# Kernel tuning notes

Measured on AMD Instinct MI355X. Metric: run time of the kernel, lower is better.

The kernel has to match this reference:

```python
import jax, jax.numpy as jnp
import numpy as np

B, C, N, T, H = 4, 128, 512, 16, 4
DK = C // H
SCALE = float(np.sqrt(DK) * 1.0)  # dk**0.5 * max(tau,1e-6), tau=1.0


def setup_inputs() -> dict:
    key = jax.random.key(0)
    ks = jax.random.split(key, 6)
    x = jax.random.normal(ks[0], (B, C, N, T), jnp.float32)
    Wq = jax.random.normal(ks[1], (C, C), jnp.float32) * (1.0 / np.sqrt(C))
    Wk = jax.random.normal(ks[2], (C, C), jnp.float32) * (1.0 / np.sqrt(C))
    # original init is identity; add tiny noise so it's not degenerate
    structural = jnp.eye(N, dtype=jnp.float32) + 0.01 * jax.random.normal(ks[3], (N, N), jnp.float32)
    fusion_w = jax.random.normal(ks[4], (2,), jnp.float32) * 0.5  # 1x1 conv over 2 input channels
    fusion_b = (jax.random.normal(ks[5], (), jnp.float32) * 0.1)
    return {"x": x, "Wq": Wq, "Wk": Wk, "structural": structural,
            "fusion_w": fusion_w, "fusion_b": fusion_b}


def reference(x, Wq, Wk, structural, fusion_w, fusion_b):
    # x: [B, C, N, T]. 1x1 conv == per-channel linear; arrange to [B,T,N,H,DK]
    Q = jnp.einsum('oc,bcnt->btno', Wq, x).reshape(B, T, N, H, DK)
    K = jnp.einsum('oc,bcnt->btno', Wk, x).reshape(B, T, N, H, DK)
    # scores: [B, T, H, N, N]
    scores = jnp.einsum('btnhd,btmhd->bthnm', Q, K) / SCALE
    att_node = jax.nn.softmax(scores, axis=-1).mean(axis=(1, 2))  # [B, N, N]
    att_struct = jax.nn.softmax(structural, axis=-1)              # [N, N]
    # fusion conv (1x1, 2->1 channels) == weighted sum + bias
    fused = fusion_w[0] * att_node + fusion_w[1] * att_struct[None] + fusion_b
    fused = 0.5 * (fused + jnp.swapaxes(fused, 1, 2))  # symmetrize
    fused = jax.nn.softmax(fused, axis=-1)             # normalize='softmax'
    x_bt = jnp.transpose(x, (0, 3, 2, 1))              # [B, T, N, C]
    x_att = jnp.einsum('bij,btjc->btic', fused, x_bt)  # weighted aggregation over nodes
    return jnp.transpose(x_att, (0, 3, 2, 1))          # [B, C, N, T]
```

## Files before the change

### kernel.cpp

```cpp
#include <hip/hip_runtime.h>

#define GPART 8
#define INV_SCALE 0.17677669529663687f
#define SMEM_SZ 36864

typedef __attribute__((ext_vector_type(8))) short bf16x8;
typedef __attribute__((ext_vector_type(4))) float f32x4;

__device__ __forceinline__ unsigned int pk2bf(float a, float b) {
  unsigned int ua = __float_as_uint(a);
  ua = (ua + 0x7FFFu + ((ua >> 16) & 1u)) >> 16;
  unsigned int ub = __float_as_uint(b);
  ub = (ub + 0x7FFFu + ((ub >> 16) & 1u)) >> 16;
  return ua | (ub << 16);
}
__device__ __forceinline__ ushort cv1(float f) {
  unsigned int u = __float_as_uint(f);
  return (ushort)((u + 0x7FFFu + ((u >> 16) & 1u)) >> 16);
}
__device__ __forceinline__ unsigned int pkfast(float a, float b) {
  unsigned int au = __float_as_uint(a) + 0x8000u;
  unsigned int bu = __float_as_uint(b) + 0x8000u;
  return __builtin_amdgcn_perm(bu, au, 0x07060302u);
}
__device__ __forceinline__ float bf2f(ushort v) {
  return __uint_as_float((unsigned int)v << 16);
}

__device__ __forceinline__ float blk_max(float v, float* red, int tid) {
#pragma unroll
  for (int off = 32; off > 0; off >>= 1) v = fmaxf(v, __shfl_xor(v, off, 64));
  if ((tid & 63) == 0) red[tid >> 6] = v;
  __syncthreads();
  v = fmaxf(fmaxf(red[0], red[1]), fmaxf(red[2], red[3]));
  __syncthreads();
  return v;
}
__device__ __forceinline__ float blk_sum(float v, float* red, int tid) {
#pragma unroll
  for (int off = 32; off > 0; off >>= 1) v += __shfl_xor(v, off, 64);
  if ((tid & 63) == 0) red[tid >> 6] = v;
  __syncthreads();
  v = (red[0] + red[1]) + (red[2] + red[3]);
  __syncthreads();
  return v;
}

__global__ __launch_bounds__(256) void k_ph1(const float* __restrict__ x,
                                             const float* __restrict__ Wq,
                                             const float* __restrict__ Wk,
                                             const float* __restrict__ S,
                                             ushort* __restrict__ Qb,
                                             ushort* __restrict__ Kb,
                                             float* __restrict__ st) {
  __shared__ __align__(16) char smem[SMEM_SZ];
  float* xl = (float*)smem;
  const int bid = blockIdx.x;
  const int b = bid >> 7;
  const int nt0 = (bid & 127) * 64;
  const int nq = nt0 >> 4;
  const int tid = threadIdx.x;
  const int w = tid >> 6, lane = tid & 63;
  const int lm = lane & 15, quad = lane >> 4;

  const float* xb = x + (size_t)b * 1048576 + nt0;
#pragma unroll
  for (int L = tid * 4; L < 8192; L += 1024) {
    int c = L >> 6, j = L & 63;
    float4 v = *(const float4*)(xb + c * 8192 + j);
    float2* dp = (float2*)(xl + c * 66 + j);
    dp[0] = make_float2(v.x, v.y);
    dp[1] = make_float2(v.z, v.w);
  }

  const int o0 = w * 32;
  bf16x8 aq[2][4], ak[2][4];
#pragma unroll
  for (int ot = 0; ot < 2; ++ot)
#pragma unroll
    for (int kc = 0; kc < 4; ++kc) {
      const int off = (o0 + ot * 16 + lm) * 128 + kc * 32 + quad * 8;
      const float4 q1 = *(const float4*)(Wq + off);
      const float4 q2 = *(const float4*)(Wq + off + 4);
      const float4 k1 = *(const float4*)(Wk + off);
      const float4 k2 = *(const float4*)(Wk + off + 4);
      union { uint4 u; bf16x8 v; } cq, ck;
      cq.u.x = pk2bf(q1.x * INV_SCALE, q1.y * INV_SCALE);
      cq.u.y = pk2bf(q1.z * INV_SCALE, q1.w * INV_SCALE);
      cq.u.z = pk2bf(q2.x * INV_SCALE, q2.y * INV_SCALE);
      cq.u.w = pk2bf(q2.z * INV_SCALE, q2.w * INV_SCALE);
      ck.u.x = pk2bf(k1.x, k1.y);
      ck.u.y = pk2bf(k1.z, k1.w);
      ck.u.z = pk2bf(k2.x, k2.y);
      ck.u.w = pk2bf(k2.z, k2.w);
      aq[ot][kc] = cq.v;
      ak[ot][kc] = ck.v;
    }
  __syncthreads();

#pragma unroll
  for (int jtl = 0; jtl < 4; ++jtl) {
    bf16x8 bfr[4];
#pragma unroll
    for (int kc = 0; kc < 4; ++kc) {
      const float* sp = xl + (kc * 32 + quad * 8) * 66 + jtl * 16 + lm;
      float f0 = sp[0],   f1 = sp[66],  f2 = sp[132], f3 = sp[198];
      float f4 = sp[264], f5 = sp[330], f6 = sp[396], f7 = sp[462];
      union { uint4 u; bf16x8 v; } cv;
      cv.u.x = pkfast(f0, f1);
      cv.u.y = pkfast(f2, f3);
      cv.u.z = pkfast(f4, f5);
      cv.u.w = pkfast(f6, f7);
      bfr[kc] = cv.v;
    }

    f32x4 accq0 = {0,0,0,0}, accq1 = {0,0,0,0};
    f32x4 acck0 = {0,0,0,0}, acck1 = {0,0,0,0};
#pragma unroll
    for (int kc = 0; kc < 4; ++kc) {
      accq0 = __builtin_amdgcn_mfma_f32_16x16x32_bf16(aq[0][kc], bfr[kc], accq0, 0, 0, 0);
      accq1 = __builtin_amdgcn_mfma_f32_16x16x32_bf16(aq[1][kc], bfr[kc], accq1, 0, 0, 0);
      acck0 = __builtin_amdgcn_mfma_f32_16x16x32_bf16(ak[0][kc], bfr[kc], acck0, 0, 0, 0);
      acck1 = __builtin_amdgcn_mfma_f32_16x16x32_bf16(ak[1][kc], bfr[kc], acck1, 0, 0, 0);
    }

    const size_t base = (size_t)b * 1048576 + (size_t)lm * 65536 + w * 16384 +
                        (size_t)(nq + jtl) * 32 + quad * 4;
    uint2 uq0, uq1, uk0, uk1;
    uq0.x = pk2bf(accq0[0], accq0[1]); uq0.y = pk2bf(accq0[2], accq0[3]);
    uq1.x = pk2bf(accq1[0], accq1[1]); uq1.y = pk2bf(accq1[2], accq1[3]);
    uk0.x = pk2bf(acck0[0], acck0[1]); uk0.y = pk2bf(acck0[2], acck0[3]);
    uk1.x = pk2bf(acck1[0], acck1[1]); uk1.y = pk2bf(acck1[2], acck1[3]);
    *(uint2*)(Qb + base)      = uq0;
    *(uint2*)(Qb + base + 16) = uq1;
    *(uint2*)(Kb + base)      = uk0;
    *(uint2*)(Kb + base + 16) = uk1;
  }

  {
    float* red = (float*)(smem + 34816);
    __syncthreads();
    const int i = bid;
    float s0 = S[i * 512 + tid], s1 = S[i * 512 + tid + 256];
    float m = blk_max(fmaxf(s0, s1), red, tid);
    float e0 = __expf(s0 - m), e1 = __expf(s1 - m);
    float sum = blk_sum(e0 + e1, red, tid);
    float inv = 1.0f / sum;
    st[i * 512 + tid] = e0 * inv;
    st[i * 512 + tid + 256] = e1 * inv;
  }
}

__global__ __launch_bounds__(256, 4) void k_ph2(const ushort* __restrict__ Qb,
                                                const ushort* __restrict__ Kb,
                                                ushort* __restrict__ part) {
  __shared__ float SH[16 * 516];
  __shared__ float red[2][4][16];
  const int strip = blockIdx.x, g = blockIdx.y, b = blockIdx.z;
  const int tid = threadIdx.x;
  const int w = tid >> 6, lane = tid & 63;
  const int lm = lane & 15, quad = lane >> 4;
  const int n0 = strip * 16;
  const int wcol0 = w * 128;

  float acc[32];
#pragma unroll
  for (int i = 0; i < 32; ++i) acc[i] = 0.f;

  for (int pi = 0; pi < 8; ++pi) {
    const int p = (g << 3) + pi;
    const size_t base = (size_t)((b * 16 + (p >> 2)) * 4 + (p & 3)) * 16384;
    bf16x8 afrag = *(const bf16x8*)(Qb + base + (size_t)(n0 + lm) * 32 + quad * 8);
    bf16x8 bfr[8];
#pragma unroll
    for (int ct = 0; ct < 8; ++ct)
      bfr[ct] = *(const bf16x8*)(Kb + base + (size_t)(wcol0 + ct * 16 + lm) * 32 + quad * 8);

    f32x4 d[8];
#pragma unroll
    for (int ct = 0; ct < 8; ++ct) {
      f32x4 z = {0.f, 0.f, 0.f, 0.f};
      d[ct] = __builtin_amdgcn_mfma_f32_16x16x32_bf16(afrag, bfr[ct], z, 0, 0, 0);
    }

    float cur[32];
    float rp0 = 0.f, rp1 = 0.f, rp2 = 0.f, rp3 = 0.f;
#pragma unroll
    for (int ct = 0; ct < 8; ++ct) {
      float e0 = __expf(d[ct][0]);
      float e1 = __expf(d[ct][1]);
      float e2 = __expf(d[ct][2]);
      float e3 = __expf(d[ct][3]);
      cur[ct * 4 + 0] = e0; cur[ct * 4 + 1] = e1;
      cur[ct * 4 + 2] = e2; cur[ct * 4 + 3] = e3;
      rp0 += e0; rp1 += e1; rp2 += e2; rp3 += e3;
    }
#pragma unroll
    for (int m = 1; m < 16; m <<= 1) {
      rp0 += __shfl_xor(rp0, m);
      rp1 += __shfl_xor(rp1, m);
      rp2 += __shfl_xor(rp2, m);
      rp3 += __shfl_xor(rp3, m);
    }
    if (lm == 0) {
      red[pi & 1][w][quad * 4 + 0] = rp0;
      red[pi & 1][w][quad * 4 + 1] = rp1;
      red[pi & 1][w][quad * 4 + 2] = rp2;
      red[pi & 1][w][quad * 4 + 3] = rp3;
    }
    __syncthreads();
#pragma unroll
    for (int r = 0; r < 4; ++r) {
      float rs = red[pi & 1][0][quad * 4 + r] + red[pi & 1][1][quad * 4 + r] +
                 red[pi & 1][2][quad * 4 + r] + red[pi & 1][3][quad * 4 + r];
      float inv = 1.0f / rs;
#pragma unroll
      for (int ct = 0; ct < 8; ++ct)
        acc[ct * 4 + r] = fmaf(cur[ct * 4 + r], inv, acc[ct * 4 + r]);
    }
  }

#pragma unroll
  for (int ct = 0; ct < 8; ++ct) {
#pragma unroll
    for (int r = 0; r < 4; ++r)
      SH[(quad * 4 + r) * 516 + wcol0 + ct * 16 + lm] = acc[ct * 4 + r];
  }
  __syncthreads();
  const int row = tid >> 4, colb = (tid & 15) * 4;
  ushort* po = part + ((size_t)((g * 4 + b) * 512 + n0 + row)) * 512 + colb;
#pragma unroll
  for (int k = 0; k < 8; ++k) {
    f32x4 v = *(const f32x4*)(SH + row * 516 + colb + k * 64);
    uint2 u;
    u.x = pk2bf(v[0], v[1]);
    u.y = pk2bf(v[2], v[3]);
    *(uint2*)(po + k * 64) = u;
  }
}

__global__ __launch_bounds__(256) void k_ph3(const float* __restrict__ x,
                                             ushort* __restrict__ xtb,
                                             const ushort* __restrict__ part,
                                             float* __restrict__ Ssym,
                                             float* __restrict__ st) {
  __shared__ __align__(16) char smem[SMEM_SZ];
  const int bid = blockIdx.x;
  const int tid = threadIdx.x;

  {
    ushort* xs = (ushort*)smem;
    const int c = bid & 127, b = bid >> 7;
    const float* in = x + ((size_t)b * 128 + c) * 8192;
    ushort* outp = xtb + ((size_t)b * 128 + c) * 8192;
#pragma unroll
    for (int it = 0; it < 8; ++it) {
      int idx = (tid + it * 256) * 4;
      int j = idx >> 4, t0 = idx & 15;
      float4 v = *(const float4*)(in + idx);
      xs[(t0 + 0) * 520 + j] = cv1(v.x);
      xs[(t0 + 1) * 520 + j] = cv1(v.y);
      xs[(t0 + 2) * 520 + j] = cv1(v.z);
      xs[(t0 + 3) * 520 + j] = cv1(v.w);
    }
    __syncthreads();
#pragma unroll
    for (int it = 0; it < 4; ++it) {
      int u = (tid + it * 256) * 8;
      int t = u >> 9, j0 = u & 511;
      *(uint4*)(outp + u) = *(const uint4*)(xs + t * 520 + j0);
    }
  }
  __syncthreads();

  if (bid < 180) {
    float* L1 = (float*)smem;
    float* L2 = L1 + 64 * 68;
    const int z = bid / 36;
    int rem = bid % 36, ti = 0;
    for (;;) { int cnt = 8 - ti; if (rem < cnt) break; rem -= cnt; ++ti; }
    const int tj = ti + rem;
    const bool diag = (ti == tj);
    const int rr = tid >> 2, cc = (tid & 3) * 16;

    float a1[16], a2[16];
#pragma unroll
    for (int k = 0; k < 16; ++k) { a1[k] = 0.f; a2[k] = 0.f; }

    if (z == 4) {
      const float* p1 = st + (ti * 64 + rr) * 512 + tj * 64 + cc;
      const float* p2 = st + (tj * 64 + rr) * 512 + ti * 64 + cc;
#pragma unroll
      for (int q = 0; q < 4; ++q) {
        float4 v = *(const float4*)(p1 + q * 4);
        a1[q * 4 + 0] = v.x; a1[q * 4 + 1] = v.y;
        a1[q * 4 + 2] = v.z; a1[q * 4 + 3] = v.w;
        if (!diag) {
          float4 u = *(const float4*)(p2 + q * 4);
          a2[q * 4 + 0] = u.x; a2[q * 4 + 1] = u.y;
          a2[q * 4 + 2] = u.z; a2[q * 4 + 3] = u.w;
        }
      }
    } else {
      const int b = z;
#pragma unroll
      for (int g = 0; g < GPART; ++g) {
        const ushort* p1 = part + ((size_t)((g * 4 + b) * 512 + ti * 64 + rr)) * 512 + tj * 64 + cc;
        const ushort* p2 = part + ((size_t)((g * 4 + b) * 512 + tj * 64 + rr)) * 512 + ti * 64 + cc;
#pragma unroll
        for (int q = 0; q < 4; ++q) {
          ushort4 v = *(const ushort4*)(p1 + q * 4);
          a1[q * 4 + 0] += bf2f(v.x); a1[q * 4 + 1] += bf2f(v.y);
          a1[q * 4 + 2] += bf2f(v.z); a1[q * 4 + 3] += bf2f(v.w);
          if (!diag) {
            ushort4 u = *(const ushort4*)(p2 + q * 4);
            a2[q * 4 + 0] += bf2f(u.x); a2[q * 4 + 1] += bf2f(u.y);
            a2[q * 4 + 2] += bf2f(u.z); a2[q * 4 + 3] += bf2f(u.w);
          }
        }
      }
    }

#pragma unroll
    for (int q = 0; q < 4; ++q) {
      *(float4*)(L1 + rr * 68 + cc + q * 4) =
          make_float4(a1[q * 4], a1[q * 4 + 1], a1[q * 4 + 2], a1[q * 4 + 3]);
      if (!diag)
        *(float4*)(L2 + rr * 68 + cc + q * 4) =
            make_float4(a2[q * 4], a2[q * 4 + 1], a2[q * 4 + 2], a2[q * 4 + 3]);
    }
    __syncthreads();

    float* M = (z < 4) ? (Ssym + (size_t)z * 262144) : st;
    const float* LT = diag ? L1 : L2;
#pragma unroll
    for (int q = 0; q < 4; ++q) {
      const int c = cc + q * 4;
      float4 o;
      o.x = L1[rr * 68 + c + 0] + LT[(c + 0) * 68 + rr];
      o.y = L1[rr * 68 + c + 1] + LT[(c + 1) * 68 + rr];
      o.z = L1[rr * 68 + c + 2] + LT[(c + 2) * 68 + rr];
      o.w = L1[rr * 68 + c + 3] + LT[(c + 3) * 68 + rr];
      *(float4*)(M + (ti * 64 + rr) * 512 + tj * 64 + c) = o;
    }
    if (!diag) {
#pragma unroll
      for (int q = 0; q < 4; ++q) {
        const int c = cc + q * 4;
        float4 o;
        o.x = L2[rr * 68 + c + 0] + L1[(c + 0) * 68 + rr];
        o.y = L2[rr * 68 + c + 1] + L1[(c + 1) * 68 + rr];
        o.z = L2[rr * 68 + c + 2] + L1[(c + 2) * 68 + rr];
        o.w = L2[rr * 68 + c + 3] + L1[(c + 3) * 68 + rr];
        *(float4*)(M + (tj * 64 + rr) * 512 + ti * 64 + c) = o;
      }
    }
  }
}

__global__ __launch_bounds__(256) void k_ph4(const float* __restrict__ Ssym,
                                             const float* __restrict__ st,
                                             const float* __restrict__ fw,
                                             const float* __restrict__ fb,
                                             ushort* __restrict__ fusedb) {
  __shared__ float red[4];
  const int i = blockIdx.x, tid = threadIdx.x;
  const float w0s = fw[0] * (0.5f / 64.f);
  const float w1s = fw[1] * 0.5f;
  const float bias = fb[0];
  float2 s2 = *(const float2*)(st + (size_t)i * 512 + tid * 2);
  for (int b = 0; b < 4; ++b) {
    const float* A = Ssym + (size_t)b * 262144 + (size_t)i * 512;
    float2 a2 = *(const float2*)(A + tid * 2);
    float l0 = fmaf(w0s, a2.x, fmaf(w1s, s2.x, bias));
    float l1 = fmaf(w0s, a2.y, fmaf(w1s, s2.y, bias));
    float m = blk_max(fmaxf(l0, l1), red, tid);
    float e0 = __expf(l0 - m), e1 = __expf(l1 - m);
    float sum = blk_sum(e0 + e1, red, tid);
    float inv = 1.0f / sum;
    *(unsigned int*)(fusedb + ((size_t)(b * 512 + i)) * 512 + tid * 2) =
        pk2bf(e0 * inv, e1 * inv);
  }
}

__global__ __launch_bounds__(256) void k_ph5(const ushort* __restrict__ fusedb,
                                             const ushort* __restrict__ xtb,
                                             float* __restrict__ out) {
  __shared__ ushort xs[16 * 520];
  const int cg = blockIdx.x;
  const int i0 = blockIdx.y * 64;
  const int b = blockIdx.z;
  const int tid = threadIdx.x, w = tid >> 6, lane = tid & 63;
  const int lm = lane & 15, quad = lane >> 4;

  const ushort* fr = fusedb + ((size_t)(b * 512 + i0 + w * 16 + lm)) * 512 + quad * 8;
  bf16x8 af[16];
#pragma unroll
  for (int kk = 0; kk < 16; ++kk) af[kk] = *(const bf16x8*)(fr + kk * 32);

  const ushort* xg = xtb + ((size_t)b * 128 + cg * 8) * 8192;
  uint4 rg[4];
#pragma unroll
  for (int it = 0; it < 4; ++it) rg[it] = *(const uint4*)(xg + (tid + it * 256) * 8);

  for (int c = 0; c < 8; ++c) {
#pragma unroll
    for (int it = 0; it < 4; ++it) {
      int u = (tid + it * 256) * 8;
      int t = u >> 9, j0 = u & 511;
      *(uint4*)(xs + t * 520 + j0) = rg[it];
    }
    __syncthreads();
    if (c < 7) {
      const ushort* xg2 = xg + (size_t)(c + 1) * 8192;
#pragma unroll
      for (int it = 0; it < 4; ++it) rg[it] = *(const uint4*)(xg2 + (tid + it * 256) * 8);
    }
    f32x4 acc = {0.f, 0.f, 0.f, 0.f};
#pragma unroll
    for (int kk = 0; kk < 16; ++kk) {
      bf16x8 bf = *(const bf16x8*)(xs + lm * 520 + kk * 32 + quad * 8);
      acc = __builtin_amdgcn_mfma_f32_16x16x32_bf16(af[kk], bf, acc, 0, 0, 0);
    }
    float* op = out + (size_t)b * 1048576 + (size_t)(cg * 8 + c) * 8192 +
                (size_t)(i0 + w * 16 + quad * 4) * 16 + lm;
    op[0]  = acc[0];
    op[16] = acc[1];
    op[32] = acc[2];
    op[48] = acc[3];
    __syncthreads();
  }
}

extern "C" void kernel_launch(void* const* d_in, const int* in_sizes, int n_in,
                              void* d_out, int out_size, void* d_ws, size_t ws_size,
                              hipStream_t stream) {
  const float* x  = (const float*)d_in[0];
  const float* Wq = (const float*)d_in[1];
  const float* Wk = (const float*)d_in[2];
  const float* S  = (const float*)d_in[3];
  const float* fw = (const float*)d_in[4];
  const float* fb = (const float*)d_in[5];
  float* out = (float*)d_out;

  ushort* Qb   = (ushort*)d_ws;
  ushort* Kb   = Qb + 4194304;
  ushort* part = Kb + 4194304;
  ushort* xtb  = Qb;
  float* Ssym  = (float*)(part + 8388608);
  float* st    = Ssym + 1048576;
  ushort* fusedb = (ushort*)(st + 262144);

  k_ph1<<<dim3(512),          256, 0, stream>>>(x, Wq, Wk, S, Qb, Kb, st);
  k_ph2<<<dim3(32, GPART, 4), 256, 0, stream>>>(Qb, Kb, part);
  k_ph3<<<dim3(512),          256, 0, stream>>>(x, xtb, part, Ssym, st);
  k_ph4<<<dim3(512),          256, 0, stream>>>(Ssym, st, fw, fb, fusedb);
  k_ph5<<<dim3(16, 8, 4),     256, 0, stream>>>(fusedb, xtb, out);
}
```

Measured before the change: 163.6 us.

## Fuse fusion-softmax into aggregation GEMM and move x transpose into score kernel

The x-to-bf16 transpose moves from the symmetrize kernel into the score-partials kernel, so the symmetrize kernel now launches only its 180 needed blocks. The separate fusion-softmax kernel is removed. The aggregation kernel now computes exp of the fused logits directly into its bf16 MFMA A-fragments. It normalizes each output row by the reciprocal row sum after the GEMM, and skips the max subtraction because the logits are small. This saves one launch and the bf16 fused-matrix round trip through memory. In exchange, every channel-group block re-reads the fp32 Ssym and st rows and recomputes the exps, a 16x redundancy that will mostly hit L2.

```diff
diff --git a/kernel.cpp b/kernel.cpp
--- a/kernel.cpp
+++ b/kernel.cpp
@@ -153,13 +153,43 @@
 
 __global__ __launch_bounds__(256, 4) void k_ph2(const ushort* __restrict__ Qb,
                                                 const ushort* __restrict__ Kb,
+                                                const float* __restrict__ x,
+                                                ushort* __restrict__ xtb,
                                                 ushort* __restrict__ part) {
-  __shared__ float SH[16 * 516];
-  __shared__ float red[2][4][16];
+  __shared__ __align__(16) char smem[SMEM_SZ];
   const int strip = blockIdx.x, g = blockIdx.y, b = blockIdx.z;
+  const int flat = strip + 32 * g + 256 * b;
   const int tid = threadIdx.x;
   const int w = tid >> 6, lane = tid & 63;
   const int lm = lane & 15, quad = lane >> 4;
+
+  if (flat < 512) {
+    ushort* xs = (ushort*)smem;
+    const int cc = flat & 127, bc = flat >> 7;
+    const float* in = x + ((size_t)bc * 128 + cc) * 8192;
+    ushort* outp = xtb + ((size_t)bc * 128 + cc) * 8192;
+#pragma unroll
+    for (int it = 0; it < 8; ++it) {
+      int idx = (tid + it * 256) * 4;
+      int j = idx >> 4, t0 = idx & 15;
+      float4 v = *(const float4*)(in + idx);
+      xs[(t0 + 0) * 520 + j] = cv1(v.x);
+      xs[(t0 + 1) * 520 + j] = cv1(v.y);
+      xs[(t0 + 2) * 520 + j] = cv1(v.z);
+      xs[(t0 + 3) * 520 + j] = cv1(v.w);
+    }
+    __syncthreads();
+#pragma unroll
+    for (int it = 0; it < 4; ++it) {
+      int u = (tid + it * 256) * 8;
+      int t = u >> 9, j0 = u & 511;
+      *(uint4*)(outp + u) = *(const uint4*)(xs + t * 520 + j0);
+    }
+  }
+  __syncthreads();
+
+  float* SH = (float*)smem;
+  float (*red)[4][16] = (float(*)[4][16])(smem + 33024);
   const int n0 = strip * 16;
   const int wcol0 = w * 128;
 
@@ -239,164 +269,142 @@
   }
 }
 
-__global__ __launch_bounds__(256) void k_ph3(const float* __restrict__ x,
-                                             ushort* __restrict__ xtb,
-                                             const ushort* __restrict__ part,
+__global__ __launch_bounds__(256) void k_ph3(const ushort* __restrict__ part,
                                              float* __restrict__ Ssym,
                                              float* __restrict__ st) {
   __shared__ __align__(16) char smem[SMEM_SZ];
   const int bid = blockIdx.x;
   const int tid = threadIdx.x;
-
-  {
-    ushort* xs = (ushort*)smem;
-    const int c = bid & 127, b = bid >> 7;
-    const float* in = x + ((size_t)b * 128 + c) * 8192;
-    ushort* outp = xtb + ((size_t)b * 128 + c) * 8192;
-#pragma unroll
-    for (int it = 0; it < 8; ++it) {
-      int idx = (tid + it * 256) * 4;
-      int j = idx >> 4, t0 = idx & 15;
-      float4 v = *(const float4*)(in + idx);
-      xs[(t0 + 0) * 520 + j] = cv1(v.x);
-      xs[(t0 + 1) * 520 + j] = cv1(v.y);
-      xs[(t0 + 2) * 520 + j] = cv1(v.z);
-      xs[(t0 + 3) * 520 + j] = cv1(v.w);
-    }
-    __syncthreads();
-#pragma unroll
-    for (int it = 0; it < 4; ++it) {
-      int u = (tid + it * 256) * 8;
-      int t = u >> 9, j0 = u & 511;
-      *(uint4*)(outp + u) = *(const uint4*)(xs + t * 520 + j0);
-    }
-  }
-  __syncthreads();
-
-  if (bid < 180) {
-    float* L1 = (float*)smem;
-    float* L2 = L1 + 64 * 68;
-    const int z = bid / 36;
-    int rem = bid % 36, ti = 0;
-    for (;;) { int cnt = 8 - ti; if (rem < cnt) break; rem -= cnt; ++ti; }
-    const int tj = ti + rem;
-    const bool diag = (ti == tj);
-    const int rr = tid >> 2, cc = (tid & 3) * 16;
-
-    float a1[16], a2[16];
-#pragma unroll
-    for (int k = 0; k < 16; ++k) { a1[k] = 0.f; a2[k] = 0.f; }
-
-    if (z == 4) {
-      const float* p1 = st + (ti * 64 + rr) * 512 + tj * 64 + cc;
-      const float* p2 = st + (tj * 64 + rr) * 512 + ti * 64 + cc;
+  float* L1 = (float*)smem;
+  float* L2 = L1 + 64 * 68;
+  const int z = bid / 36;
+  int rem = bid % 36, ti = 0;
+  for (;;) { int cnt = 8 - ti; if (rem < cnt) break; rem -= cnt; ++ti; }
+  const int tj = ti + rem;
+  const bool diag = (ti == tj);
+  const int rr = tid >> 2, cc = (tid & 3) * 16;
+
+  float a1[16], a2[16];
+#pragma unroll
+  for (int k = 0; k < 16; ++k) { a1[k] = 0.f; a2[k] = 0.f; }
+
+  if (z == 4) {
+    const float* p1 = st + (ti * 64 + rr) * 512 + tj * 64 + cc;
+    const float* p2 = st + (tj * 64 + rr) * 512 + ti * 64 + cc;
+#pragma unroll
+    for (int q = 0; q < 4; ++q) {
+      float4 v = *(const float4*)(p1 + q * 4);
+      a1[q * 4 + 0] = v.x; a1[q * 4 + 1] = v.y;
+      a1[q * 4 + 2] = v.z; a1[q * 4 + 3] = v.w;
+      if (!diag) {
+        float4 u = *(const float4*)(p2 + q * 4);
+        a2[q * 4 + 0] = u.x; a2[q * 4 + 1] = u.y;
+        a2[q * 4 + 2] = u.z; a2[q * 4 + 3] = u.w;
+      }
+    }
+  } else {
+    const int b = z;
+#pragma unroll
+    for (int g = 0; g < GPART; ++g) {
+      const ushort* p1 = part + ((size_t)((g * 4 + b) * 512 + ti * 64 + rr)) * 512 + tj * 64 + cc;
+      const ushort* p2 = part + ((size_t)((g * 4 + b) * 512 + tj * 64 + rr)) * 512 + ti * 64 + cc;
 #pragma unroll
       for (int q = 0; q < 4; ++q) {
-        float4 v = *(const float4*)(p1 + q * 4);
-        a1[q * 4 + 0] = v.x; a1[q * 4 + 1] = v.y;
-        a1[q * 4 + 2] = v.z; a1[q * 4 + 3] = v.w;
+        ushort4 v = *(const ushort4*)(p1 + q * 4);
+        a1[q * 4 + 0] += bf2f(v.x); a1[q * 4 + 1] += bf2f(v.y);
+        a1[q * 4 + 2] += bf2f(v.z); a1[q * 4 + 3] += bf2f(v.w);
         if (!diag) {
-          float4 u = *(const float4*)(p2 + q * 4);
-          a2[q * 4 + 0] = u.x; a2[q * 4 + 1] = u.y;
-          a2[q * 4 + 2] = u.z; a2[q * 4 + 3] = u.w;
+          ushort4 u = *(const ushort4*)(p2 + q * 4);
+          a2[q * 4 + 0] += bf2f(u.x); a2[q * 4 + 1] += bf2f(u.y);
+          a2[q * 4 + 2] += bf2f(u.z); a2[q * 4 + 3] += bf2f(u.w);
         }
       }
-    } else {
-      const int b = z;
-#pragma unroll
-      for (int g = 0; g < GPART; ++g) {
-        const ushort* p1 = part + ((size_t)((g * 4 + b) * 512 + ti * 64 + rr)) * 512 + tj * 64 + cc;
-        const ushort* p2 = part + ((size_t)((g * 4 + b) * 512 + tj * 64 + rr)) * 512 + ti * 64 + cc;
-#pragma unroll
-        for (int q = 0; q < 4; ++q) {
-          ushort4 v = *(const ushort4*)(p1 + q * 4);
-          a1[q * 4 + 0] += bf2f(v.x); a1[q * 4 + 1] += bf2f(v.y);
-          a1[q * 4 + 2] += bf2f(v.z); a1[q * 4 + 3] += bf2f(v.w);
-          if (!diag) {
-            ushort4 u = *(const ushort4*)(p2 + q * 4);
-            a2[q * 4 + 0] += bf2f(u.x); a2[q * 4 + 1] += bf2f(u.y);
-            a2[q * 4 + 2] += bf2f(u.z); a2[q * 4 + 3] += bf2f(u.w);
-          }
-        }
-      }
-    }
-
-#pragma unroll
-    for (int q = 0; q < 4; ++q) {
-      *(float4*)(L1 + rr * 68 + cc + q * 4) =
-          make_float4(a1[q * 4], a1[q * 4 + 1], a1[q * 4 + 2], a1[q * 4 + 3]);
-      if (!diag)
-        *(float4*)(L2 + rr * 68 + cc + q * 4) =
-            make_float4(a2[q * 4], a2[q * 4 + 1], a2[q * 4 + 2], a2[q * 4 + 3]);
-    }
-    __syncthreads();
-
-    float* M = (z < 4) ? (Ssym + (size_t)z * 262144) : st;
-    const float* LT = diag ? L1 : L2;
+    }
+  }
+
+#pragma unroll
+  for (int q = 0; q < 4; ++q) {
+    *(float4*)(L1 + rr * 68 + cc + q * 4) =
+        make_float4(a1[q * 4], a1[q * 4 + 1], a1[q * 4 + 2], a1[q * 4 + 3]);
+    if (!diag)
+      *(float4*)(L2 + rr * 68 + cc + q * 4) =
+          make_float4(a2[q * 4], a2[q * 4 + 1], a2[q * 4 + 2], a2[q * 4 + 3]);
+  }
+  __syncthreads();
+
+  float* M = (z < 4) ? (Ssym + (size_t)z * 262144) : st;
+  const float* LT = diag ? L1 : L2;
+#pragma unroll
+  for (int q = 0; q < 4; ++q) {
+    const int c = cc + q * 4;
+    float4 o;
+    o.x = L1[rr * 68 + c + 0] + LT[(c + 0) * 68 + rr];
+    o.y = L1[rr * 68 + c + 1] + LT[(c + 1) * 68 + rr];
+    o.z = L1[rr * 68 + c + 2] + LT[(c + 2) * 68 + rr];
+    o.w = L1[rr * 68 + c + 3] + LT[(c + 3) * 68 + rr];
+    *(float4*)(M + (ti * 64 + rr) * 512 + tj * 64 + c) = o;
+  }
+  if (!diag) {
 #pragma unroll
     for (int q = 0; q < 4; ++q) {
       const int c = cc + q * 4;
       float4 o;
-      o.x = L1[rr * 68 + c + 0] + LT[(c + 0) * 68 + rr];
-      o.y = L1[rr * 68 + c + 1] + LT[(c + 1) * 68 + rr];
-      o.z = L1[rr * 68 + c + 2] + LT[(c + 2) * 68 + rr];
-      o.w = L1[rr * 68 + c + 3] + LT[(c + 3) * 68 + rr];
-      *(float4*)(M + (ti * 64 + rr) * 512 + tj * 64 + c) = o;
-    }
-    if (!diag) {
-#pragma unroll
-      for (int q = 0; q < 4; ++q) {
-        const int c = cc + q * 4;
-        float4 o;
-        o.x = L2[rr * 68 + c + 0] + L1[(c + 0) * 68 + rr];
-        o.y = L2[rr * 68 + c + 1] + L1[(c + 1) * 68 + rr];
-        o.z = L2[rr * 68 + c + 2] + L1[(c + 2) * 68 + rr];
-        o.w = L2[rr * 68 + c + 3] + L1[(c + 3) * 68 + rr];
-        *(float4*)(M + (tj * 64 + rr) * 512 + ti * 64 + c) = o;
-      }
-    }
-  }
-}
-
-__global__ __launch_bounds__(256) void k_ph4(const float* __restrict__ Ssym,
+      o.x = L2[rr * 68 + c + 0] + L1[(c + 0) * 68 + rr];
+      o.y = L2[rr * 68 + c + 1] + L1[(c + 1) * 68 + rr];
+      o.z = L2[rr * 68 + c + 2] + L1[(c + 2) * 68 + rr];
+      o.w = L2[rr * 68 + c + 3] + L1[(c + 3) * 68 + rr];
+      *(float4*)(M + (tj * 64 + rr) * 512 + ti * 64 + c) = o;
+    }
+  }
+}
+
+__global__ __launch_bounds__(256) void k_ph5(const float* __restrict__ Ssym,
                                              const float* __restrict__ st,
                                              const float* __restrict__ fw,
                                              const float* __restrict__ fb,
-                                             ushort* __restrict__ fusedb) {
-  __shared__ float red[4];
-  const int i = blockIdx.x, tid = threadIdx.x;
-  const float w0s = fw[0] * (0.5f / 64.f);
-  const float w1s = fw[1] * 0.5f;
-  const float bias = fb[0];
-  float2 s2 = *(const float2*)(st + (size_t)i * 512 + tid * 2);
-  for (int b = 0; b < 4; ++b) {
-    const float* A = Ssym + (size_t)b * 262144 + (size_t)i * 512;
-    float2 a2 = *(const float2*)(A + tid * 2);
-    float l0 = fmaf(w0s, a2.x, fmaf(w1s, s2.x, bias));
-    float l1 = fmaf(w0s, a2.y, fmaf(w1s, s2.y, bias));
-    float m = blk_max(fmaxf(l0, l1), red, tid);
-    float e0 = __expf(l0 - m), e1 = __expf(l1 - m);
-    float sum = blk_sum(e0 + e1, red, tid);
-    float inv = 1.0f / sum;
-    *(unsigned int*)(fusedb + ((size_t)(b * 512 + i)) * 512 + tid * 2) =
-        pk2bf(e0 * inv, e1 * inv);
-  }
-}
-
-__global__ __launch_bounds__(256) void k_ph5(const ushort* __restrict__ fusedb,
                                              const ushort* __restrict__ xtb,
                                              float* __restrict__ out) {
   __shared__ ushort xs[16 * 520];
+  __shared__ float inv64[64];
   const int cg = blockIdx.x;
   const int i0 = blockIdx.y * 64;
   const int b = blockIdx.z;
   const int tid = threadIdx.x, w = tid >> 6, lane = tid & 63;
   const int lm = lane & 15, quad = lane >> 4;
-
-  const ushort* fr = fusedb + ((size_t)(b * 512 + i0 + w * 16 + lm)) * 512 + quad * 8;
+  const float w0s = fw[0] * (0.5f / 64.f);
+  const float w1s = fw[1] * 0.5f;
+  const float bias = fb[0];
+
+  const int rowi = i0 + w * 16 + lm;
+  const float* As = Ssym + (size_t)b * 262144 + (size_t)rowi * 512 + quad * 8;
+  const float* Ss = st + (size_t)rowi * 512 + quad * 8;
   bf16x8 af[16];
-#pragma unroll
-  for (int kk = 0; kk < 16; ++kk) af[kk] = *(const bf16x8*)(fr + kk * 32);
+  float rowsum = 0.f;
+#pragma unroll
+  for (int kk = 0; kk < 16; ++kk) {
+    float4 a1 = *(const float4*)(As + kk * 32);
+    float4 a2 = *(const float4*)(As + kk * 32 + 4);
+    float4 s1 = *(const float4*)(Ss + kk * 32);
+    float4 s2 = *(const float4*)(Ss + kk * 32 + 4);
+    float e0 = __expf(fmaf(w0s, a1.x, fmaf(w1s, s1.x, bias)));
+    float e1 = __expf(fmaf(w0s, a1.y, fmaf(w1s, s1.y, bias)));
+    float e2 = __expf(fmaf(w0s, a1.z, fmaf(w1s, s1.z, bias)));
+    float e3 = __expf(fmaf(w0s, a1.w, fmaf(w1s, s1.w, bias)));
+    float e4 = __expf(fmaf(w0s, a2.x, fmaf(w1s, s2.x, bias)));
+    float e5 = __expf(fmaf(w0s, a2.y, fmaf(w1s, s2.y, bias)));
+    float e6 = __expf(fmaf(w0s, a2.z, fmaf(w1s, s2.z, bias)));
+    float e7 = __expf(fmaf(w0s, a2.w, fmaf(w1s, s2.w, bias)));
+    rowsum += ((e0 + e1) + (e2 + e3)) + ((e4 + e5) + (e6 + e7));
+    union { uint4 u; bf16x8 v; } cv;
+    cv.u.x = pk2bf(e0, e1);
+    cv.u.y = pk2bf(e2, e3);
+    cv.u.z = pk2bf(e4, e5);
+    cv.u.w = pk2bf(e6, e7);
+    af[kk] = cv.v;
+  }
+  rowsum += __shfl_xor(rowsum, 16);
+  rowsum += __shfl_xor(rowsum, 32);
+  if (quad == 0) inv64[w * 16 + lm] = 1.0f / rowsum;
 
   const ushort* xg = xtb + ((size_t)b * 128 + cg * 8) * 8192;
   uint4 rg[4];
@@ -422,12 +430,13 @@
       bf16x8 bf = *(const bf16x8*)(xs + lm * 520 + kk * 32 + quad * 8);
       acc = __builtin_amdgcn_mfma_f32_16x16x32_bf16(af[kk], bf, acc, 0, 0, 0);
     }
+    const int rb = w * 16 + quad * 4;
     float* op = out + (size_t)b * 1048576 + (size_t)(cg * 8 + c) * 8192 +
-                (size_t)(i0 + w * 16 + quad * 4) * 16 + lm;
-    op[0]  = acc[0];
-    op[16] = acc[1];
-    op[32] = acc[2];
-    op[48] = acc[3];
+                (size_t)(i0 + rb) * 16 + lm;
+    op[0]  = acc[0] * inv64[rb + 0];
+    op[16] = acc[1] * inv64[rb + 1];
+    op[32] = acc[2] * inv64[rb + 2];
+    op[48] = acc[3] * inv64[rb + 3];
     __syncthreads();
   }
 }
@@ -446,14 +455,12 @@
   ushort* Qb   = (ushort*)d_ws;
   ushort* Kb   = Qb + 4194304;
   ushort* part = Kb + 4194304;
-  ushort* xtb  = Qb;
-  float* Ssym  = (float*)(part + 8388608);
-  float* st    = Ssym + 1048576;
-  ushort* fusedb = (ushort*)(st + 262144);
+  ushort* xtb  = part + 8388608;
+  float* Ssym  = (float*)(xtb + 4194304);
+  float* st    = Ssym + 4194304;
 
   k_ph1<<<dim3(512),          256, 0, stream>>>(x, Wq, Wk, S, Qb, Kb, st);
-  k_ph2<<<dim3(32, GPART, 4), 256, 0, stream>>>(Qb, Kb, part);
-  k_ph3<<<dim3(512),          256, 0, stream>>>(x, xtb, part, Ssym, st);
-  k_ph4<<<dim3(512),          256, 0, stream>>>(Ssym, st, fw, fb, fusedb);
-  k_ph5<<<dim3(16, 8, 4),     256, 0, stream>>>(fusedb, xtb, out);
-}
+  k_ph2<<<dim3(32, GPART, 4), 256, 0, stream>>>(Qb, Kb, x, xtb, part);
+  k_ph3<<<dim3(180),          256, 0, stream>>>(part, Ssym, st);
+  k_ph5<<<dim3(16, 8, 4),     256, 0, stream>>>(Ssym, st, fw, fb, xtb, out);
+}
```

Measured after the change: 166.4 us. About the same (+1.7%).
